# Optimization experiments

Hardware: AMD Instinct MI355X
Metric: run time of the kernel (lower is better)

The kernel has to match this reference:

```python
import jax, jax.numpy as jnp
import numpy as np

SX, SY, C, K = 256, 256, 3, 15
DD, DT, SIGMA = 5, 0.2, 0.65
C0 = tuple(i % C for i in range(K))
C1 = tuple(tuple(i for i in range(K) if i % C == c) for c in range(C))
MA = DD - SIGMA  # flow magnitude bound


def _sobel(A):
    # A: (X, Y, c) -> (X, Y, 2, c); matches jsp.signal.convolve2d(..., mode='same')
    kx = jnp.array([[1., 0., -1.], [2., 0., -2.], [1., 0., -1.]], dtype=A.dtype)
    ky = kx.T
    # convolve2d flips the kernel; emulate true convolution by correlating with rot180 kernels
    kern = jnp.stack([jnp.rot90(ky, 2), jnp.rot90(kx, 2)])[:, None]  # (2,1,3,3): [grad_y, grad_x]
    x = jnp.transpose(A, (2, 0, 1))[:, None]                          # (c,1,X,Y)
    out = jax.lax.conv_general_dilated(x, kern, (1, 1), 'SAME')       # (c,2,X,Y)
    return jnp.transpose(out, (2, 3, 1, 0))                           # (X,Y,2,c)


def _reintegration(A, P, F):
    # Reintegration tracking, has_hidden=True, border='wall', mix='softmax'
    xs, ys = jnp.meshgrid(jnp.arange(SX), jnp.arange(SY))
    pos = (jnp.dstack((ys, xs)) + .5).astype(A.dtype)     # (X,Y,2) cell centers (row, col)
    mus = pos[..., None] + jnp.clip(DT * F, -MA, MA)      # (X,Y,2,C) target centers
    mus = jnp.clip(mus, SIGMA, SX - SIGMA)                # wall border
    shifts = jnp.array([(dx, dy) for dx in range(-DD, DD + 1) for dy in range(-DD, DD + 1)])
    cap = min(1., 2 * SIGMA)

    def step(sft):
        sh = (sft[0], sft[1])
        Ar = jnp.roll(A, sh, axis=(0, 1))
        Pr = jnp.roll(P, sh, axis=(0, 1))
        mur = jnp.roll(mus, sh, axis=(0, 1))
        dpmu = jnp.abs(pos[..., None] - mur)              # (X,Y,2,C)
        sz = .5 - dpmu + SIGMA
        area = jnp.prod(jnp.clip(sz, 0., cap), axis=2) / (4 * SIGMA ** 2)  # (X,Y,C)
        return Ar * area, Pr

    nA, nP = jax.vmap(step)(shifts)                       # (N,X,Y,C), (N,X,Y,K)
    expnA = jnp.exp(nA.sum(-1, keepdims=True)) - 1.       # softmax mix rule
    newA = nA.sum(0)
    newP = (nP * expnA).sum(0) / (expnA.sum(0) + 1e-10)
    return newA, newP


def _forward(A, P, fK_real, fK_imag, m, s):
    fK = fK_real + 1j * fK_imag                           # (X,Y,K) kernel FFTs
    fA = jnp.fft.fft2(A, axes=(0, 1))                     # (X,Y,C)
    fAk = jnp.take(fA, jnp.array(C0), axis=2)             # (X,Y,K) per-kernel source channel
    U = jnp.real(jnp.fft.ifft2(fK * fAk, axes=(0, 1)))    # (X,Y,K)
    U = (2. * jnp.exp(-((U - m) ** 2) / (2. * s ** 2)) - 1.) * P  # growth(U,m,s)*P
    U = jnp.dstack([U[:, :, C1[c]].sum(-1) for c in range(C)])    # (X,Y,C)
    F = _sobel(U)                                         # (X,Y,2,C)
    Cg = _sobel(A.sum(-1, keepdims=True))                 # (X,Y,2,1)
    alpha = jnp.clip((A[:, :, None, :] / 2.) ** 2, 0., 1.)
    F = jnp.clip(F * (1. - alpha) - Cg * alpha, -MA, MA)
    return _reintegration(A, P, F)


def setup_inputs() -> dict:
    key = jax.random.key(0)
    kA, kP, kr, km, ks, ka, kb, kw = jax.random.split(key, 8)
    A = jax.random.uniform(kA, (SX, SY, C), dtype=jnp.float32)
    P = jax.random.uniform(kP, (SX, SY, K), dtype=jnp.float32)
    R = 15.0
    r = jax.random.uniform(kr, (K,), minval=.2, maxval=1.)
    m = jax.random.uniform(km, (K,), minval=.05, maxval=.5, dtype=jnp.float32)
    s = jax.random.uniform(ks, (K,), minval=.001, maxval=.18, dtype=jnp.float32)
    a = jax.random.uniform(ka, (K, 3))
    b = jax.random.uniform(kb, (K, 3), minval=.001, maxval=1.)
    w = jax.random.uniform(kw, (K, 3), minval=.01, maxval=.5)
    mid = SX // 2
    D = jnp.linalg.norm(jnp.mgrid[-mid:mid, -mid:mid], axis=0)[..., None] / ((R + 15.) * r)  # (X,Y,K)
    Kk = jax.nn.sigmoid(-(D - 1.) * 10.) * (b * jnp.exp(-((D[..., None] - a) / w) ** 2)).sum(-1)
    nK = Kk / Kk.sum((0, 1), keepdims=True)
    fK = jnp.fft.fft2(jnp.fft.fftshift(nK, axes=(0, 1)), axes=(0, 1))
    return {"A": A, "P": P,
            "fK_real": jnp.real(fK).astype(jnp.float32),
            "fK_imag": jnp.imag(fK).astype(jnp.float32),
            "m": m, "s": s}


def reference(A, P, fK_real, fK_imag, m, s):
    return _forward(A, P, fK_real, fK_imag, m, s)
```

## Files before the change

kernel.cpp:

```cpp
#include <hip/hip_runtime.h>


#define XY  65536
#define NC  3
#define NK  15
#define WPAD 260
#define RW  136

__device__ __forceinline__ float2 cmul(float2 a, float2 b) {
  return make_float2(a.x * b.x - a.y * b.y, a.x * b.y + a.y * b.x);
}

__device__ __forceinline__ int swz(int i) { return i ^ ((i >> 4) & 15); }

__device__ __forceinline__ void wave_fence() {
  asm volatile("" ::: "memory");
  __builtin_amdgcn_wave_barrier();
  asm volatile("" ::: "memory");
}

__device__ __forceinline__ void fft256_wave(float2* b0, float2* b1, int t, float sign) {
  float2* src = b0;
  float2* dst = b1;
#pragma unroll
  for (int stage = 0; stage < 4; ++stage) {
    wave_fence();
    const int Ns = 1 << (2 * stage);
    float2 v0 = src[swz(t)];
    float2 v1 = src[swz(t + 64)];
    float2 v2 = src[swz(t + 128)];
    float2 v3 = src[swz(t + 192)];
    const int jm = t & (Ns - 1);
    float ang = sign * 6.283185307179586f * (float)jm / (float)(Ns * 4);
    float sn, cs;
    __sincosf(ang, &sn, &cs);
    float2 w1 = make_float2(cs, sn);
    float2 w2 = cmul(w1, w1);
    float2 w3 = cmul(w2, w1);
    v1 = cmul(v1, w1);
    v2 = cmul(v2, w2);
    v3 = cmul(v3, w3);
    float2 a0 = make_float2(v0.x + v2.x, v0.y + v2.y);
    float2 a1 = make_float2(v0.x - v2.x, v0.y - v2.y);
    float2 a2 = make_float2(v1.x + v3.x, v1.y + v3.y);
    float2 a3 = make_float2(v1.x - v3.x, v1.y - v3.y);
    float2 ia3 = make_float2(-sign * a3.y, sign * a3.x);
    const int idxD = ((t >> (2 * stage)) << (2 * stage)) * 4 + jm;
    dst[swz(idxD)]          = make_float2(a0.x + a2.x, a0.y + a2.y);
    dst[swz(idxD + Ns)]     = make_float2(a1.x + ia3.x, a1.y + ia3.y);
    dst[swz(idxD + 2 * Ns)] = make_float2(a0.x - a2.x, a0.y - a2.y);
    dst[swz(idxD + 3 * Ns)] = make_float2(a1.x - ia3.x, a1.y - ia3.y);
    float2* tmp = src; src = dst; dst = tmp;
  }
  wave_fence();
}

__global__ __launch_bounds__(256) void k_rowfft(const float* __restrict__ A,
                                                float2* __restrict__ RF) {
  __shared__ float2 l0[4 * WPAD], l1[4 * WPAD];
  const int tid = threadIdx.x;
  const int w = tid >> 6, lane = tid & 63;
  const int c = blockIdx.x >> 6;
  const int x = ((blockIdx.x & 63) << 2) + w;
  float2* b0 = l0 + w * WPAD;
  float2* b1 = l1 + w * WPAD;
#pragma unroll
  for (int r = 0; r < 4; ++r) {
    int y = lane + 64 * r;
    b0[swz(y)] = make_float2(A[(x * 256 + y) * NC + c], 0.0f);
  }
  fft256_wave(b0, b1, lane, -1.0f);
  float2* dst = RF + (c * 256 + x) * RW;
#pragma unroll
  for (int r = 0; r < 2; ++r) {
    int y = lane + 64 * r;
    dst[y] = b0[swz(y)];
  }
  if (lane < 8) {
    dst[128 + lane] = (lane == 0) ? b0[swz(128)] : make_float2(0.f, 0.f);
  }
}

__global__ __launch_bounds__(512, 1) void k_colfft(const float* __restrict__ fKr,
                                                   const float* __restrict__ fKi,
                                                   const float2* __restrict__ RF,
                                                   float2* __restrict__ T2) {
  __shared__ float2 lds0[8 * WPAD];
  __shared__ float2 lds1[8 * WPAD];
  const int tid = threadIdx.x;
  const int k = blockIdx.x / 17;
  const int tile = blockIdx.x - k * 17;
  const int y0 = (tile < 16) ? (tile << 3) : 128;
  const int c = k % 3;
  const int w = tid >> 6, lane = tid & 63;
  const int y = y0 + w;

  float2 Kv[4];
#pragma unroll
  for (int r = 0; r < 4; ++r) {
    const int xx = lane + 64 * r;
    const int fi = (xx * 256 + y) * NK + k;
    Kv[r] = make_float2(fKr[fi], fKi[fi]);
  }

  {
    const int q = tid & 3;
#pragma unroll
    for (int r = 0; r < 2; ++r) {
      const int x = (tid >> 2) + (r << 7);
      const float4* src = (const float4*)(RF + (c * 256 + x) * RW + y0);
      float4 v = src[q];
      lds0[(2 * q) * WPAD + swz(x)]     = make_float2(v.x, v.y);
      lds0[(2 * q + 1) * WPAD + swz(x)] = make_float2(v.z, v.w);
    }
  }
  __syncthreads();

  float2* b0 = lds0 + w * WPAD;
  float2* b1 = lds1 + w * WPAD;
  fft256_wave(b0, b1, lane, -1.0f);

  float2 fa[4];
#pragma unroll
  for (int r = 0; r < 4; ++r) fa[r] = b0[swz(lane + 64 * r)];
#pragma unroll
  for (int r = 0; r < 4; ++r) {
    const int x = lane + 64 * r;
    b0[swz(x)] = cmul(Kv[r], fa[r]);
  }
  fft256_wave(b0, b1, lane, 1.0f);
  __syncthreads();

  {
    const int q = tid & 3;
#pragma unroll
    for (int r = 0; r < 2; ++r) {
      const int x = (tid >> 2) + (r << 7);
      float2 v0 = lds0[(2 * q) * WPAD + swz(x)];
      float2 v1 = lds0[(2 * q + 1) * WPAD + swz(x)];
      float4* dst = (float4*)(T2 + (k * 256 + x) * RW + y0);
      dst[q] = make_float4(v0.x, v0.y, v1.x, v1.y);
    }
  }
}

__global__ __launch_bounds__(320, 1) void k_irowfft_growth(const float2* __restrict__ T2,
                                                           const float* __restrict__ P,
                                                           const float* __restrict__ m,
                                                           const float* __restrict__ s,
                                                           float* __restrict__ Ucol) {
  __shared__ float2 lds0[5 * WPAD];
  __shared__ float2 lds1[5 * WPAD];
  __shared__ float accs[5 * WPAD];
  const int tid = threadIdx.x;
  const int x = blockIdx.x & 255;
  const int c = blockIdx.x >> 8;
  const int j = tid >> 6, lane = tid & 63;
  const int k = c + 3 * j;

  float pv[4];
#pragma unroll
  for (int r = 0; r < 4; ++r) {
    int y = lane + 64 * r;
    pv[r] = P[(x * 256 + y) * NK + k];
  }
  const float mk = m[k];
  const float sk = s[k];
  const float inv2s2 = 0.5f / (sk * sk);

  float2* b0 = lds0 + j * WPAD;
  float2* b1 = lds1 + j * WPAD;
  const float2* src = T2 + (k * 256 + x) * RW;
#pragma unroll
  for (int r = 0; r < 2; ++r) {
    int y = lane + 64 * r;
    float2 v = src[y];
    b0[swz(y)] = v;
    if (y > 0) b0[swz(256 - y)] = make_float2(v.x, -v.y);
  }
  if (lane == 0) b0[swz(128)] = src[128];
  fft256_wave(b0, b1, lane, 1.0f);

#pragma unroll
  for (int r = 0; r < 4; ++r) {
    int y = lane + 64 * r;
    float U = b0[swz(y)].x * (1.0f / 65536.0f);
    float d = U - mk;
    float g = 2.0f * __expf(-d * d * inv2s2) - 1.0f;
    accs[j * WPAD + y] = g * pv[r];
  }
  __syncthreads();
  if (tid < 256) {
    float sum = 0.f;
#pragma unroll
    for (int j2 = 0; j2 < 5; ++j2) sum += accs[j2 * WPAD + tid];
    Ucol[c * XY + x * 256 + tid] = sum;
  }
}

__global__ __launch_bounds__(256) void k_flow_reint(const float* __restrict__ A,
                                                    const float* __restrict__ P,
                                                    const float* __restrict__ Ucol,
                                                    float* __restrict__ outA,
                                                    float* __restrict__ outP) {
  __shared__ float4 lAF[484];
  __shared__ float4 lU[484];
  __shared__ float4 lF[2][400];
  __shared__ float4 lP[4][400];
  const int tid = threadIdx.x;
  const int x0 = (blockIdx.x >> 4) << 4;
  const int y0 = (blockIdx.x & 15) << 4;
  const float MA = 4.35f;
  const float SIGMA = 0.65f;
  const float INV4S2 = 1.0f / (4.0f * 0.65f * 0.65f);
  const float DT = 0.2f;

  for (int cell = tid; cell < 484; cell += 256) {
    const int r = cell / 22, cc = cell - r * 22;
    const int sx = (x0 + r - 3) & 255;
    const int sy = (y0 + cc - 3) & 255;
    const int sb = sx * 256 + sy;
    const float* ap = A + sb * NC;
    const float a0 = ap[0], a1 = ap[1], a2 = ap[2];
    lAF[cell] = make_float4(a0, a1, a2, a0 + a1 + a2);
    lU[cell] = make_float4(Ucol[sb], Ucol[XY + sb], Ucol[2 * XY + sb], 0.f);
  }
  for (int cell = tid; cell < 400; cell += 256) {
    const int r = cell / 20, cc = cell - r * 20;
    const int sx = (x0 + r - 2) & 255;
    const int sy = (y0 + cc - 2) & 255;
    const float* pp = P + (sx * 256 + sy) * NK;
    lP[0][cell] = make_float4(pp[0], pp[1], pp[2], pp[3]);
    lP[1][cell] = make_float4(pp[4], pp[5], pp[6], pp[7]);
    lP[2][cell] = make_float4(pp[8], pp[9], pp[10], pp[11]);
    lP[3][cell] = make_float4(pp[12], pp[13], pp[14], 0.f);
  }
  __syncthreads();

  for (int cell = tid; cell < 400; cell += 256) {
    const int fr = cell / 20, fc = cell - fr * 20;
    const int sx = (x0 + fr - 2) & 255;
    const int sy = (y0 + fc - 2) & 255;
    float u[3][3][3];
    float as[3][3];
#pragma unroll
    for (int di = -1; di <= 1; ++di) {
#pragma unroll
      for (int dj = -1; dj <= 1; ++dj) {
        const bool zb = (sx == 0 && di < 0) || (sx == 255 && di > 0) ||
                        (sy == 0 && dj < 0) || (sy == 255 && dj > 0);
        float4 uv = make_float4(0.f, 0.f, 0.f, 0.f);
        float av = 0.f;
        if (!zb) {
          const int lc = (fr + 1 + di) * 22 + (fc + 1 + dj);
          uv = lU[lc];
          av = lAF[lc].w;
        }
        u[0][di + 1][dj + 1] = uv.x;
        u[1][di + 1][dj + 1] = uv.y;
        u[2][di + 1][dj + 1] = uv.z;
        as[di + 1][dj + 1] = av;
      }
    }
    const float cg0 = (as[2][0] + 2.f * as[2][1] + as[2][2]) -
                      (as[0][0] + 2.f * as[0][1] + as[0][2]);
    const float cg1 = (as[0][2] + 2.f * as[1][2] + as[2][2]) -
                      (as[0][0] + 2.f * as[1][0] + as[2][0]);
    const float4 ac = lAF[(fr + 1) * 22 + (fc + 1)];
    float fo[2][3];
#pragma unroll
    for (int c = 0; c < NC; ++c) {
      float f0 = (u[c][2][0] + 2.f * u[c][2][1] + u[c][2][2]) -
                 (u[c][0][0] + 2.f * u[c][0][1] + u[c][0][2]);
      float f1 = (u[c][0][2] + 2.f * u[c][1][2] + u[c][2][2]) -
                 (u[c][0][0] + 2.f * u[c][1][0] + u[c][2][0]);
      const float a = (c == 0) ? ac.x : (c == 1) ? ac.y : ac.z;
      const float ah = a * 0.5f;
      const float al = fminf(ah * ah, 1.0f);
      fo[0][c] = fminf(fmaxf(f0 * (1.f - al) - cg0 * al, -MA), MA);
      fo[1][c] = fminf(fmaxf(f1 * (1.f - al) - cg1 * al, -MA), MA);
    }
    lF[0][cell] = make_float4(fo[0][0], fo[0][1], fo[0][2], fo[1][0]);
    lF[1][cell] = make_float4(fo[1][1], fo[1][2], 0.f, 0.f);
  }
  __syncthreads();

  const int lx = tid >> 4, ly = tid & 15;
  const int x = x0 + lx, y = y0 + ly;
  const float px = x + 0.5f;
  const float py = y + 0.5f;

  float accA0 = 0.f, accA1 = 0.f, accA2 = 0.f;
  float accP[15];
#pragma unroll
  for (int k = 0; k < NK; ++k) accP[k] = 0.f;
  float esum = 0.f;

#pragma unroll
  for (int dx = -2; dx <= 2; ++dx) {
#pragma unroll
    for (int dy = -2; dy <= 2; ++dy) {
      const int lc = (lx + 2 - dx) * 20 + (ly + 2 - dy);
      const int la = (lx + 3 - dx) * 22 + (ly + 3 - dy);
      const int sx = (x - dx) & 255;
      const int sy = (y - dy) & 255;
      const float spx = sx + 0.5f;
      const float spy = sy + 0.5f;
      const float4 av = lAF[la];
      const float4 fv0 = lF[0][lc];
      const float4 fv1 = lF[1][lc];
      float mu0 = fminf(fmaxf(spx + DT * fv0.x, SIGMA), 256.f - SIGMA);
      float mu1 = fminf(fmaxf(spy + DT * fv0.w, SIGMA), 256.f - SIGMA);
      float sz0 = fminf(fmaxf(0.5f - fabsf(px - mu0) + SIGMA, 0.f), 1.f);
      float sz1 = fminf(fmaxf(0.5f - fabsf(py - mu1) + SIGMA, 0.f), 1.f);
      float na0 = av.x * (sz0 * sz1 * INV4S2);
      mu0 = fminf(fmaxf(spx + DT * fv0.y, SIGMA), 256.f - SIGMA);
      mu1 = fminf(fmaxf(spy + DT * fv1.x, SIGMA), 256.f - SIGMA);
      sz0 = fminf(fmaxf(0.5f - fabsf(px - mu0) + SIGMA, 0.f), 1.f);
      sz1 = fminf(fmaxf(0.5f - fabsf(py - mu1) + SIGMA, 0.f), 1.f);
      float na1 = av.y * (sz0 * sz1 * INV4S2);
      mu0 = fminf(fmaxf(spx + DT * fv0.z, SIGMA), 256.f - SIGMA);
      mu1 = fminf(fmaxf(spy + DT * fv1.y, SIGMA), 256.f - SIGMA);
      sz0 = fminf(fmaxf(0.5f - fabsf(px - mu0) + SIGMA, 0.f), 1.f);
      sz1 = fminf(fmaxf(0.5f - fabsf(py - mu1) + SIGMA, 0.f), 1.f);
      float na2 = av.z * (sz0 * sz1 * INV4S2);

      const float e = __expf(na0 + na1 + na2) - 1.0f;
      accA0 += na0; accA1 += na1; accA2 += na2;
      esum += e;
      const float4 p0 = lP[0][lc];
      const float4 p1 = lP[1][lc];
      const float4 p2 = lP[2][lc];
      const float4 p3 = lP[3][lc];
      accP[0]  += p0.x * e; accP[1]  += p0.y * e; accP[2]  += p0.z * e; accP[3]  += p0.w * e;
      accP[4]  += p1.x * e; accP[5]  += p1.y * e; accP[6]  += p1.z * e; accP[7]  += p1.w * e;
      accP[8]  += p2.x * e; accP[9]  += p2.y * e; accP[10] += p2.z * e; accP[11] += p2.w * e;
      accP[12] += p3.x * e; accP[13] += p3.y * e; accP[14] += p3.z * e;
    }
  }

  const int b = x * 256 + y;
  outA[b * NC + 0] = accA0;
  outA[b * NC + 1] = accA1;
  outA[b * NC + 2] = accA2;
  const float inv = 1.0f / (esum + 1e-10f);
#pragma unroll
  for (int k = 0; k < NK; ++k) outP[b * NK + k] = accP[k] * inv;
}

extern "C" void kernel_launch(void* const* d_in, const int* in_sizes, int n_in,
                              void* d_out, int out_size, void* d_ws, size_t ws_size,
                              hipStream_t stream) {
  const float* A   = (const float*)d_in[0];
  const float* P   = (const float*)d_in[1];
  const float* fKr = (const float*)d_in[2];
  const float* fKi = (const float*)d_in[3];
  const float* m   = (const float*)d_in[4];
  const float* s   = (const float*)d_in[5];

  float* ws = (float*)d_ws;
  float2* RF   = (float2*)ws;
  float2* T2   = RF + NC * 256 * RW;
  float*  Ucol = (float*)(T2 + NK * 256 * RW);

  float* outA = (float*)d_out;
  float* outP = outA + NC * XY;

  k_rowfft<<<NC * 64, 256, 0, stream>>>(A, RF);
  k_colfft<<<NK * 17, 512, 0, stream>>>(fKr, fKi, RF, T2);
  k_irowfft_growth<<<NC * 256, 320, 0, stream>>>(T2, P, m, s, Ucol);
  k_flow_reint<<<256, 256, 0, stream>>>(A, P, Ucol, outA, outP);
}
```

Baseline: 99.65 us.

## Fuse four kernels into one cooperative persistent kernel with grid syncs

Merges the row FFT, column FFT with kernel multiply, inverse row FFT with growth, and flow/reintegration stages into a single cooperative kernel of 256 blocks of 512 threads, separated by grid-wide syncs. This removes three kernel launch gaps and inter-kernel drain/fill. The cost is reduced per-stage parallelism: each stage now uses fewer blocks or leaves waves idle (e.g. only 3 of 8 waves work in the row FFT, half the threads in the reintegration loop), and the grid syncs add their own overhead.

```diff
diff --git a/kernel.cpp b/kernel.cpp
--- a/kernel.cpp
+++ b/kernel.cpp
@@ -1,4 +1,7 @@
 #include <hip/hip_runtime.h>
+#include <hip/hip_cooperative_groups.h>
+
+namespace cg = cooperative_groups;
 
 
 #define XY  65536
@@ -55,297 +58,300 @@
   wave_fence();
 }
 
-__global__ __launch_bounds__(256) void k_rowfft(const float* __restrict__ A,
-                                                float2* __restrict__ RF) {
-  __shared__ float2 l0[4 * WPAD], l1[4 * WPAD];
+__global__ __launch_bounds__(512, 1) void k_mega(const float* __restrict__ A,
+                                                 const float* __restrict__ P,
+                                                 const float* __restrict__ fKr,
+                                                 const float* __restrict__ fKi,
+                                                 const float* __restrict__ m,
+                                                 const float* __restrict__ s,
+                                                 float2* __restrict__ RF,
+                                                 float2* __restrict__ T2,
+                                                 float* __restrict__ Ucol,
+                                                 float* __restrict__ outA,
+                                                 float* __restrict__ outP) {
+  __shared__ union {
+    struct { float2 l0[8 * WPAD], l1[8 * WPAD]; } fft;
+    struct { float2 l0[8 * WPAD], l1[8 * WPAD]; float accs[15 * WPAD]; } p3;
+    struct { float4 lAF[484], lU[484], lF[2 * 400], lP[4 * 400]; } p4;
+  } sm;
+  cg::grid_group grid = cg::this_grid();
   const int tid = threadIdx.x;
+  const int bid = blockIdx.x;
   const int w = tid >> 6, lane = tid & 63;
-  const int c = blockIdx.x >> 6;
-  const int x = ((blockIdx.x & 63) << 2) + w;
-  float2* b0 = l0 + w * WPAD;
-  float2* b1 = l1 + w * WPAD;
-#pragma unroll
-  for (int r = 0; r < 4; ++r) {
-    int y = lane + 64 * r;
-    b0[swz(y)] = make_float2(A[(x * 256 + y) * NC + c], 0.0f);
-  }
-  fft256_wave(b0, b1, lane, -1.0f);
-  float2* dst = RF + (c * 256 + x) * RW;
-#pragma unroll
-  for (int r = 0; r < 2; ++r) {
-    int y = lane + 64 * r;
-    dst[y] = b0[swz(y)];
-  }
-  if (lane < 8) {
-    dst[128 + lane] = (lane == 0) ? b0[swz(128)] : make_float2(0.f, 0.f);
-  }
-}
-
-__global__ __launch_bounds__(512, 1) void k_colfft(const float* __restrict__ fKr,
-                                                   const float* __restrict__ fKi,
-                                                   const float2* __restrict__ RF,
-                                                   float2* __restrict__ T2) {
-  __shared__ float2 lds0[8 * WPAD];
-  __shared__ float2 lds1[8 * WPAD];
-  const int tid = threadIdx.x;
-  const int k = blockIdx.x / 17;
-  const int tile = blockIdx.x - k * 17;
-  const int y0 = (tile < 16) ? (tile << 3) : 128;
-  const int c = k % 3;
-  const int w = tid >> 6, lane = tid & 63;
-  const int y = y0 + w;
-
-  float2 Kv[4];
-#pragma unroll
-  for (int r = 0; r < 4; ++r) {
-    const int xx = lane + 64 * r;
-    const int fi = (xx * 256 + y) * NK + k;
-    Kv[r] = make_float2(fKr[fi], fKi[fi]);
-  }
+
+  if (w < 3) {
+    const int c = w;
+    const int x = bid;
+    float2* b0 = sm.fft.l0 + w * WPAD;
+    float2* b1 = sm.fft.l1 + w * WPAD;
+#pragma unroll
+    for (int r = 0; r < 4; ++r) {
+      int y = lane + 64 * r;
+      b0[swz(y)] = make_float2(A[(x * 256 + y) * NC + c], 0.0f);
+    }
+    fft256_wave(b0, b1, lane, -1.0f);
+    float2* dst = RF + (c * 256 + x) * RW;
+#pragma unroll
+    for (int r = 0; r < 2; ++r) {
+      int y = lane + 64 * r;
+      dst[y] = b0[swz(y)];
+    }
+    if (lane < 8) {
+      dst[128 + lane] = (lane == 0) ? b0[swz(128)] : make_float2(0.f, 0.f);
+    }
+  }
+  __threadfence();
+  grid.sync();
+
+  if (bid < 255) {
+    const int k = bid / 17;
+    const int tile = bid - k * 17;
+    const int y0 = (tile < 16) ? (tile << 3) : 128;
+    const int c = k % 3;
+    const int y = y0 + w;
+
+    float2 Kv[4];
+#pragma unroll
+    for (int r = 0; r < 4; ++r) {
+      const int xx = lane + 64 * r;
+      const int fi = (xx * 256 + y) * NK + k;
+      Kv[r] = make_float2(fKr[fi], fKi[fi]);
+    }
+
+    {
+      const int q = tid & 3;
+#pragma unroll
+      for (int r = 0; r < 2; ++r) {
+        const int x = (tid >> 2) + (r << 7);
+        const float4* src = (const float4*)(RF + (c * 256 + x) * RW + y0);
+        float4 v = src[q];
+        sm.fft.l0[(2 * q) * WPAD + swz(x)]     = make_float2(v.x, v.y);
+        sm.fft.l0[(2 * q + 1) * WPAD + swz(x)] = make_float2(v.z, v.w);
+      }
+    }
+    __syncthreads();
+
+    float2* b0 = sm.fft.l0 + w * WPAD;
+    float2* b1 = sm.fft.l1 + w * WPAD;
+    fft256_wave(b0, b1, lane, -1.0f);
+
+    float2 fa[4];
+#pragma unroll
+    for (int r = 0; r < 4; ++r) fa[r] = b0[swz(lane + 64 * r)];
+#pragma unroll
+    for (int r = 0; r < 4; ++r) {
+      const int x = lane + 64 * r;
+      b0[swz(x)] = cmul(Kv[r], fa[r]);
+    }
+    fft256_wave(b0, b1, lane, 1.0f);
+    __syncthreads();
+
+    {
+      const int q = tid & 3;
+#pragma unroll
+      for (int r = 0; r < 2; ++r) {
+        const int x = (tid >> 2) + (r << 7);
+        float2 v0 = sm.fft.l0[(2 * q) * WPAD + swz(x)];
+        float2 v1 = sm.fft.l0[(2 * q + 1) * WPAD + swz(x)];
+        float4* dst = (float4*)(T2 + (k * 256 + x) * RW + y0);
+        dst[q] = make_float4(v0.x, v0.y, v1.x, v1.y);
+      }
+    }
+  }
+  __threadfence();
+  grid.sync();
 
   {
-    const int q = tid & 3;
-#pragma unroll
-    for (int r = 0; r < 2; ++r) {
-      const int x = (tid >> 2) + (r << 7);
-      const float4* src = (const float4*)(RF + (c * 256 + x) * RW + y0);
-      float4 v = src[q];
-      lds0[(2 * q) * WPAD + swz(x)]     = make_float2(v.x, v.y);
-      lds0[(2 * q + 1) * WPAD + swz(x)] = make_float2(v.z, v.w);
-    }
-  }
-  __syncthreads();
-
-  float2* b0 = lds0 + w * WPAD;
-  float2* b1 = lds1 + w * WPAD;
-  fft256_wave(b0, b1, lane, -1.0f);
-
-  float2 fa[4];
-#pragma unroll
-  for (int r = 0; r < 4; ++r) fa[r] = b0[swz(lane + 64 * r)];
-#pragma unroll
-  for (int r = 0; r < 4; ++r) {
-    const int x = lane + 64 * r;
-    b0[swz(x)] = cmul(Kv[r], fa[r]);
-  }
-  fft256_wave(b0, b1, lane, 1.0f);
-  __syncthreads();
+    const int x = bid;
+    float2* b0 = sm.p3.l0 + w * WPAD;
+    float2* b1 = sm.p3.l1 + w * WPAD;
+    for (int k = w; k < NK; k += 8) {
+      float pv[4];
+#pragma unroll
+      for (int r = 0; r < 4; ++r) {
+        int y = lane + 64 * r;
+        pv[r] = P[(x * 256 + y) * NK + k];
+      }
+      const float mk = m[k];
+      const float sk = s[k];
+      const float inv2s2 = 0.5f / (sk * sk);
+
+      const float2* src = T2 + (k * 256 + x) * RW;
+#pragma unroll
+      for (int r = 0; r < 2; ++r) {
+        int y = lane + 64 * r;
+        float2 v = src[y];
+        b0[swz(y)] = v;
+        if (y > 0) b0[swz(256 - y)] = make_float2(v.x, -v.y);
+      }
+      if (lane == 0) b0[swz(128)] = src[128];
+      fft256_wave(b0, b1, lane, 1.0f);
+
+#pragma unroll
+      for (int r = 0; r < 4; ++r) {
+        int y = lane + 64 * r;
+        float U = b0[swz(y)].x * (1.0f / 65536.0f);
+        float d = U - mk;
+        float g = 2.0f * __expf(-d * d * inv2s2) - 1.0f;
+        sm.p3.accs[k * WPAD + y] = g * pv[r];
+      }
+    }
+    __syncthreads();
+    if (tid < 256) {
+#pragma unroll
+      for (int c = 0; c < NC; ++c) {
+        float sum = 0.f;
+#pragma unroll
+        for (int j2 = 0; j2 < 5; ++j2) sum += sm.p3.accs[(c + 3 * j2) * WPAD + tid];
+        Ucol[c * XY + x * 256 + tid] = sum;
+      }
+    }
+  }
+  __threadfence();
+  grid.sync();
 
   {
-    const int q = tid & 3;
-#pragma unroll
-    for (int r = 0; r < 2; ++r) {
-      const int x = (tid >> 2) + (r << 7);
-      float2 v0 = lds0[(2 * q) * WPAD + swz(x)];
-      float2 v1 = lds0[(2 * q + 1) * WPAD + swz(x)];
-      float4* dst = (float4*)(T2 + (k * 256 + x) * RW + y0);
-      dst[q] = make_float4(v0.x, v0.y, v1.x, v1.y);
-    }
-  }
-}
-
-__global__ __launch_bounds__(320, 1) void k_irowfft_growth(const float2* __restrict__ T2,
-                                                           const float* __restrict__ P,
-                                                           const float* __restrict__ m,
-                                                           const float* __restrict__ s,
-                                                           float* __restrict__ Ucol) {
-  __shared__ float2 lds0[5 * WPAD];
-  __shared__ float2 lds1[5 * WPAD];
-  __shared__ float accs[5 * WPAD];
-  const int tid = threadIdx.x;
-  const int x = blockIdx.x & 255;
-  const int c = blockIdx.x >> 8;
-  const int j = tid >> 6, lane = tid & 63;
-  const int k = c + 3 * j;
-
-  float pv[4];
-#pragma unroll
-  for (int r = 0; r < 4; ++r) {
-    int y = lane + 64 * r;
-    pv[r] = P[(x * 256 + y) * NK + k];
-  }
-  const float mk = m[k];
-  const float sk = s[k];
-  const float inv2s2 = 0.5f / (sk * sk);
-
-  float2* b0 = lds0 + j * WPAD;
-  float2* b1 = lds1 + j * WPAD;
-  const float2* src = T2 + (k * 256 + x) * RW;
-#pragma unroll
-  for (int r = 0; r < 2; ++r) {
-    int y = lane + 64 * r;
-    float2 v = src[y];
-    b0[swz(y)] = v;
-    if (y > 0) b0[swz(256 - y)] = make_float2(v.x, -v.y);
-  }
-  if (lane == 0) b0[swz(128)] = src[128];
-  fft256_wave(b0, b1, lane, 1.0f);
-
-#pragma unroll
-  for (int r = 0; r < 4; ++r) {
-    int y = lane + 64 * r;
-    float U = b0[swz(y)].x * (1.0f / 65536.0f);
-    float d = U - mk;
-    float g = 2.0f * __expf(-d * d * inv2s2) - 1.0f;
-    accs[j * WPAD + y] = g * pv[r];
-  }
-  __syncthreads();
-  if (tid < 256) {
-    float sum = 0.f;
-#pragma unroll
-    for (int j2 = 0; j2 < 5; ++j2) sum += accs[j2 * WPAD + tid];
-    Ucol[c * XY + x * 256 + tid] = sum;
-  }
-}
-
-__global__ __launch_bounds__(256) void k_flow_reint(const float* __restrict__ A,
-                                                    const float* __restrict__ P,
-                                                    const float* __restrict__ Ucol,
-                                                    float* __restrict__ outA,
-                                                    float* __restrict__ outP) {
-  __shared__ float4 lAF[484];
-  __shared__ float4 lU[484];
-  __shared__ float4 lF[2][400];
-  __shared__ float4 lP[4][400];
-  const int tid = threadIdx.x;
-  const int x0 = (blockIdx.x >> 4) << 4;
-  const int y0 = (blockIdx.x & 15) << 4;
-  const float MA = 4.35f;
-  const float SIGMA = 0.65f;
-  const float INV4S2 = 1.0f / (4.0f * 0.65f * 0.65f);
-  const float DT = 0.2f;
-
-  for (int cell = tid; cell < 484; cell += 256) {
-    const int r = cell / 22, cc = cell - r * 22;
-    const int sx = (x0 + r - 3) & 255;
-    const int sy = (y0 + cc - 3) & 255;
-    const int sb = sx * 256 + sy;
-    const float* ap = A + sb * NC;
-    const float a0 = ap[0], a1 = ap[1], a2 = ap[2];
-    lAF[cell] = make_float4(a0, a1, a2, a0 + a1 + a2);
-    lU[cell] = make_float4(Ucol[sb], Ucol[XY + sb], Ucol[2 * XY + sb], 0.f);
-  }
-  for (int cell = tid; cell < 400; cell += 256) {
-    const int r = cell / 20, cc = cell - r * 20;
-    const int sx = (x0 + r - 2) & 255;
-    const int sy = (y0 + cc - 2) & 255;
-    const float* pp = P + (sx * 256 + sy) * NK;
-    lP[0][cell] = make_float4(pp[0], pp[1], pp[2], pp[3]);
-    lP[1][cell] = make_float4(pp[4], pp[5], pp[6], pp[7]);
-    lP[2][cell] = make_float4(pp[8], pp[9], pp[10], pp[11]);
-    lP[3][cell] = make_float4(pp[12], pp[13], pp[14], 0.f);
-  }
-  __syncthreads();
-
-  for (int cell = tid; cell < 400; cell += 256) {
-    const int fr = cell / 20, fc = cell - fr * 20;
-    const int sx = (x0 + fr - 2) & 255;
-    const int sy = (y0 + fc - 2) & 255;
-    float u[3][3][3];
-    float as[3][3];
-#pragma unroll
-    for (int di = -1; di <= 1; ++di) {
-#pragma unroll
-      for (int dj = -1; dj <= 1; ++dj) {
-        const bool zb = (sx == 0 && di < 0) || (sx == 255 && di > 0) ||
-                        (sy == 0 && dj < 0) || (sy == 255 && dj > 0);
-        float4 uv = make_float4(0.f, 0.f, 0.f, 0.f);
-        float av = 0.f;
-        if (!zb) {
-          const int lc = (fr + 1 + di) * 22 + (fc + 1 + dj);
-          uv = lU[lc];
-          av = lAF[lc].w;
+    const int x0 = (bid >> 4) << 4;
+    const int y0t = (bid & 15) << 4;
+    const float MA = 4.35f;
+    const float SIGMA = 0.65f;
+    const float INV4S2 = 1.0f / (4.0f * 0.65f * 0.65f);
+    const float DT = 0.2f;
+
+    for (int cell = tid; cell < 484; cell += 512) {
+      const int r = cell / 22, cc = cell - r * 22;
+      const int sx = (x0 + r - 3) & 255;
+      const int sy = (y0t + cc - 3) & 255;
+      const int sb = sx * 256 + sy;
+      const float* ap = A + sb * NC;
+      const float a0 = ap[0], a1 = ap[1], a2 = ap[2];
+      sm.p4.lAF[cell] = make_float4(a0, a1, a2, a0 + a1 + a2);
+      sm.p4.lU[cell] = make_float4(Ucol[sb], Ucol[XY + sb], Ucol[2 * XY + sb], 0.f);
+    }
+    for (int cell = tid; cell < 400; cell += 512) {
+      const int r = cell / 20, cc = cell - r * 20;
+      const int sx = (x0 + r - 2) & 255;
+      const int sy = (y0t + cc - 2) & 255;
+      const float* pp = P + (sx * 256 + sy) * NK;
+      sm.p4.lP[0 * 400 + cell] = make_float4(pp[0], pp[1], pp[2], pp[3]);
+      sm.p4.lP[1 * 400 + cell] = make_float4(pp[4], pp[5], pp[6], pp[7]);
+      sm.p4.lP[2 * 400 + cell] = make_float4(pp[8], pp[9], pp[10], pp[11]);
+      sm.p4.lP[3 * 400 + cell] = make_float4(pp[12], pp[13], pp[14], 0.f);
+    }
+    __syncthreads();
+
+    for (int cell = tid; cell < 400; cell += 512) {
+      const int fr = cell / 20, fc = cell - fr * 20;
+      const int sx = (x0 + fr - 2) & 255;
+      const int sy = (y0t + fc - 2) & 255;
+      float u[3][3][3];
+      float as[3][3];
+#pragma unroll
+      for (int di = -1; di <= 1; ++di) {
+#pragma unroll
+        for (int dj = -1; dj <= 1; ++dj) {
+          const bool zb = (sx == 0 && di < 0) || (sx == 255 && di > 0) ||
+                          (sy == 0 && dj < 0) || (sy == 255 && dj > 0);
+          float4 uv = make_float4(0.f, 0.f, 0.f, 0.f);
+          float av = 0.f;
+          if (!zb) {
+            const int lc = (fr + 1 + di) * 22 + (fc + 1 + dj);
+            uv = sm.p4.lU[lc];
+            av = sm.p4.lAF[lc].w;
+          }
+          u[0][di + 1][dj + 1] = uv.x;
+          u[1][di + 1][dj + 1] = uv.y;
+          u[2][di + 1][dj + 1] = uv.z;
+          as[di + 1][dj + 1] = av;
         }
-        u[0][di + 1][dj + 1] = uv.x;
-        u[1][di + 1][dj + 1] = uv.y;
-        u[2][di + 1][dj + 1] = uv.z;
-        as[di + 1][dj + 1] = av;
-      }
-    }
-    const float cg0 = (as[2][0] + 2.f * as[2][1] + as[2][2]) -
-                      (as[0][0] + 2.f * as[0][1] + as[0][2]);
-    const float cg1 = (as[0][2] + 2.f * as[1][2] + as[2][2]) -
-                      (as[0][0] + 2.f * as[1][0] + as[2][0]);
-    const float4 ac = lAF[(fr + 1) * 22 + (fc + 1)];
-    float fo[2][3];
-#pragma unroll
-    for (int c = 0; c < NC; ++c) {
-      float f0 = (u[c][2][0] + 2.f * u[c][2][1] + u[c][2][2]) -
-                 (u[c][0][0] + 2.f * u[c][0][1] + u[c][0][2]);
-      float f1 = (u[c][0][2] + 2.f * u[c][1][2] + u[c][2][2]) -
-                 (u[c][0][0] + 2.f * u[c][1][0] + u[c][2][0]);
-      const float a = (c == 0) ? ac.x : (c == 1) ? ac.y : ac.z;
-      const float ah = a * 0.5f;
-      const float al = fminf(ah * ah, 1.0f);
-      fo[0][c] = fminf(fmaxf(f0 * (1.f - al) - cg0 * al, -MA), MA);
-      fo[1][c] = fminf(fmaxf(f1 * (1.f - al) - cg1 * al, -MA), MA);
-    }
-    lF[0][cell] = make_float4(fo[0][0], fo[0][1], fo[0][2], fo[1][0]);
-    lF[1][cell] = make_float4(fo[1][1], fo[1][2], 0.f, 0.f);
-  }
-  __syncthreads();
-
-  const int lx = tid >> 4, ly = tid & 15;
-  const int x = x0 + lx, y = y0 + ly;
-  const float px = x + 0.5f;
-  const float py = y + 0.5f;
-
-  float accA0 = 0.f, accA1 = 0.f, accA2 = 0.f;
-  float accP[15];
-#pragma unroll
-  for (int k = 0; k < NK; ++k) accP[k] = 0.f;
-  float esum = 0.f;
-
-#pragma unroll
-  for (int dx = -2; dx <= 2; ++dx) {
-#pragma unroll
-    for (int dy = -2; dy <= 2; ++dy) {
-      const int lc = (lx + 2 - dx) * 20 + (ly + 2 - dy);
-      const int la = (lx + 3 - dx) * 22 + (ly + 3 - dy);
-      const int sx = (x - dx) & 255;
-      const int sy = (y - dy) & 255;
-      const float spx = sx + 0.5f;
-      const float spy = sy + 0.5f;
-      const float4 av = lAF[la];
-      const float4 fv0 = lF[0][lc];
-      const float4 fv1 = lF[1][lc];
-      float mu0 = fminf(fmaxf(spx + DT * fv0.x, SIGMA), 256.f - SIGMA);
-      float mu1 = fminf(fmaxf(spy + DT * fv0.w, SIGMA), 256.f - SIGMA);
-      float sz0 = fminf(fmaxf(0.5f - fabsf(px - mu0) + SIGMA, 0.f), 1.f);
-      float sz1 = fminf(fmaxf(0.5f - fabsf(py - mu1) + SIGMA, 0.f), 1.f);
-      float na0 = av.x * (sz0 * sz1 * INV4S2);
-      mu0 = fminf(fmaxf(spx + DT * fv0.y, SIGMA), 256.f - SIGMA);
-      mu1 = fminf(fmaxf(spy + DT * fv1.x, SIGMA), 256.f - SIGMA);
-      sz0 = fminf(fmaxf(0.5f - fabsf(px - mu0) + SIGMA, 0.f), 1.f);
-      sz1 = fminf(fmaxf(0.5f - fabsf(py - mu1) + SIGMA, 0.f), 1.f);
-      float na1 = av.y * (sz0 * sz1 * INV4S2);
-      mu0 = fminf(fmaxf(spx + DT * fv0.z, SIGMA), 256.f - SIGMA);
-      mu1 = fminf(fmaxf(spy + DT * fv1.y, SIGMA), 256.f - SIGMA);
-      sz0 = fminf(fmaxf(0.5f - fabsf(px - mu0) + SIGMA, 0.f), 1.f);
-      sz1 = fminf(fmaxf(0.5f - fabsf(py - mu1) + SIGMA, 0.f), 1.f);
-      float na2 = av.z * (sz0 * sz1 * INV4S2);
-
-      const float e = __expf(na0 + na1 + na2) - 1.0f;
-      accA0 += na0; accA1 += na1; accA2 += na2;
-      esum += e;
-      const float4 p0 = lP[0][lc];
-      const float4 p1 = lP[1][lc];
-      const float4 p2 = lP[2][lc];
-      const float4 p3 = lP[3][lc];
-      accP[0]  += p0.x * e; accP[1]  += p0.y * e; accP[2]  += p0.z * e; accP[3]  += p0.w * e;
-      accP[4]  += p1.x * e; accP[5]  += p1.y * e; accP[6]  += p1.z * e; accP[7]  += p1.w * e;
-      accP[8]  += p2.x * e; accP[9]  += p2.y * e; accP[10] += p2.z * e; accP[11] += p2.w * e;
-      accP[12] += p3.x * e; accP[13] += p3.y * e; accP[14] += p3.z * e;
-    }
-  }
-
-  const int b = x * 256 + y;
-  outA[b * NC + 0] = accA0;
-  outA[b * NC + 1] = accA1;
-  outA[b * NC + 2] = accA2;
-  const float inv = 1.0f / (esum + 1e-10f);
-#pragma unroll
-  for (int k = 0; k < NK; ++k) outP[b * NK + k] = accP[k] * inv;
+      }
+      const float cg0 = (as[2][0] + 2.f * as[2][1] + as[2][2]) -
+                        (as[0][0] + 2.f * as[0][1] + as[0][2]);
+      const float cg1 = (as[0][2] + 2.f * as[1][2] + as[2][2]) -
+                        (as[0][0] + 2.f * as[1][0] + as[2][0]);
+      const float4 ac = sm.p4.lAF[(fr + 1) * 22 + (fc + 1)];
+      float fo[2][3];
+#pragma unroll
+      for (int c = 0; c < NC; ++c) {
+        float f0 = (u[c][2][0] + 2.f * u[c][2][1] + u[c][2][2]) -
+                   (u[c][0][0] + 2.f * u[c][0][1] + u[c][0][2]);
+        float f1 = (u[c][0][2] + 2.f * u[c][1][2] + u[c][2][2]) -
+                   (u[c][0][0] + 2.f * u[c][1][0] + u[c][2][0]);
+        const float a = (c == 0) ? ac.x : (c == 1) ? ac.y : ac.z;
+        const float ah = a * 0.5f;
+        const float al = fminf(ah * ah, 1.0f);
+        fo[0][c] = fminf(fmaxf(f0 * (1.f - al) - cg0 * al, -MA), MA);
+        fo[1][c] = fminf(fmaxf(f1 * (1.f - al) - cg1 * al, -MA), MA);
+      }
+      sm.p4.lF[0 * 400 + cell] = make_float4(fo[0][0], fo[0][1], fo[0][2], fo[1][0]);
+      sm.p4.lF[1 * 400 + cell] = make_float4(fo[1][1], fo[1][2], 0.f, 0.f);
+    }
+    __syncthreads();
+
+    if (tid < 256) {
+      const int lx = tid >> 4, ly = tid & 15;
+      const int x = x0 + lx, y = y0t + ly;
+      const float px = x + 0.5f;
+      const float py = y + 0.5f;
+
+      float accA0 = 0.f, accA1 = 0.f, accA2 = 0.f;
+      float accP[15];
+#pragma unroll
+      for (int k = 0; k < NK; ++k) accP[k] = 0.f;
+      float esum = 0.f;
+
+#pragma unroll
+      for (int dx = -2; dx <= 2; ++dx) {
+#pragma unroll
+        for (int dy = -2; dy <= 2; ++dy) {
+          const int lc = (lx + 2 - dx) * 20 + (ly + 2 - dy);
+          const int la = (lx + 3 - dx) * 22 + (ly + 3 - dy);
+          const int sx = (x - dx) & 255;
+          const int sy = (y - dy) & 255;
+          const float spx = sx + 0.5f;
+          const float spy = sy + 0.5f;
+          const float4 av = sm.p4.lAF[la];
+          const float4 fv0 = sm.p4.lF[0 * 400 + lc];
+          const float4 fv1 = sm.p4.lF[1 * 400 + lc];
+          float mu0 = fminf(fmaxf(spx + DT * fv0.x, SIGMA), 256.f - SIGMA);
+          float mu1 = fminf(fmaxf(spy + DT * fv0.w, SIGMA), 256.f - SIGMA);
+          float sz0 = fminf(fmaxf(0.5f - fabsf(px - mu0) + SIGMA, 0.f), 1.f);
+          float sz1 = fminf(fmaxf(0.5f - fabsf(py - mu1) + SIGMA, 0.f), 1.f);
+          float na0 = av.x * (sz0 * sz1 * INV4S2);
+          mu0 = fminf(fmaxf(spx + DT * fv0.y, SIGMA), 256.f - SIGMA);
+          mu1 = fminf(fmaxf(spy + DT * fv1.x, SIGMA), 256.f - SIGMA);
+          sz0 = fminf(fmaxf(0.5f - fabsf(px - mu0) + SIGMA, 0.f), 1.f);
+          sz1 = fminf(fmaxf(0.5f - fabsf(py - mu1) + SIGMA, 0.f), 1.f);
+          float na1 = av.y * (sz0 * sz1 * INV4S2);
+          mu0 = fminf(fmaxf(spx + DT * fv0.z, SIGMA), 256.f - SIGMA);
+          mu1 = fminf(fmaxf(spy + DT * fv1.y, SIGMA), 256.f - SIGMA);
+          sz0 = fminf(fmaxf(0.5f - fabsf(px - mu0) + SIGMA, 0.f), 1.f);
+          sz1 = fminf(fmaxf(0.5f - fabsf(py - mu1) + SIGMA, 0.f), 1.f);
+          float na2 = av.z * (sz0 * sz1 * INV4S2);
+
+          const float e = __expf(na0 + na1 + na2) - 1.0f;
+          accA0 += na0; accA1 += na1; accA2 += na2;
+          esum += e;
+          const float4 p0 = sm.p4.lP[0 * 400 + lc];
+          const float4 p1 = sm.p4.lP[1 * 400 + lc];
+          const float4 p2 = sm.p4.lP[2 * 400 + lc];
+          const float4 p3 = sm.p4.lP[3 * 400 + lc];
+          accP[0]  += p0.x * e; accP[1]  += p0.y * e; accP[2]  += p0.z * e; accP[3]  += p0.w * e;
+          accP[4]  += p1.x * e; accP[5]  += p1.y * e; accP[6]  += p1.z * e; accP[7]  += p1.w * e;
+          accP[8]  += p2.x * e; accP[9]  += p2.y * e; accP[10] += p2.z * e; accP[11] += p2.w * e;
+          accP[12] += p3.x * e; accP[13] += p3.y * e; accP[14] += p3.z * e;
+        }
+      }
+
+      const int b = x * 256 + y;
+      outA[b * NC + 0] = accA0;
+      outA[b * NC + 1] = accA1;
+      outA[b * NC + 2] = accA2;
+      const float inv = 1.0f / (esum + 1e-10f);
+#pragma unroll
+      for (int k = 0; k < NK; ++k) outP[b * NK + k] = accP[k] * inv;
+    }
+  }
 }
 
 extern "C" void kernel_launch(void* const* d_in, const int* in_sizes, int n_in,
@@ -366,8 +372,8 @@
   float* outA = (float*)d_out;
   float* outP = outA + NC * XY;
 
-  k_rowfft<<<NC * 64, 256, 0, stream>>>(A, RF);
-  k_colfft<<<NK * 17, 512, 0, stream>>>(fKr, fKi, RF, T2);
-  k_irowfft_growth<<<NC * 256, 320, 0, stream>>>(T2, P, m, s, Ucol);
-  k_flow_reint<<<256, 256, 0, stream>>>(A, P, Ucol, outA, outP);
-}
+  void* args[] = {(void*)&A, (void*)&P, (void*)&fKr, (void*)&fKi, (void*)&m,
+                  (void*)&s, (void*)&RF, (void*)&T2, (void*)&Ucol,
+                  (void*)&outA, (void*)&outP};
+  hipLaunchCooperativeKernel((void*)k_mega, dim3(256), dim3(512), args, 0, stream);
+}
```

After: 330.5 us. +231.7%, slower.
